# Kernel tuning notes

Measured on AMD Instinct MI355X. Metric: run time of the kernel, lower is better.

## Reference

```python
import jax, jax.numpy as jnp
import numpy as np
from jax import lax

N, C, H, W = 5, 256, 128, 128
RATIO = 16
KS = 3
SIGMA = 1.0
THRE = 0.01


def _conv2d_same(x, w):
    k = w.shape[-1]
    p = (k - 1) // 2
    return lax.conv_general_dilated(x, w, (1, 1), [(p, p), (p, p)],
                                    dimension_numbers=('NCHW', 'OIHW', 'NCHW'))


def _gaussian2d():
    c = KS // 2
    x, y = np.mgrid[-c:KS - c, -c:KS - c]
    g = 1.0 / (2.0 * np.pi * SIGMA) * np.exp(-(x ** 2 + y ** 2) / (2.0 * SIGMA ** 2))
    return jnp.asarray(g, jnp.float32).reshape(1, 1, KS, KS)


def _gaussian1d():
    x = np.arange(-(KS - 1) // 2, (KS + 1) // 2, dtype=np.float32)
    g = np.exp(-x ** 2 / (2.0 * SIGMA ** 2))
    g = g / g.sum()
    return jnp.asarray(g, jnp.float32).reshape(1, 1, KS)


def setup_inputs() -> dict:
    key = jax.random.key(0)
    ks = jax.random.split(key, 12)
    s = 0.05
    return {
        'feat': jax.random.normal(ks[0], (N, C, H, W), jnp.float32),
        'mlp_w1': jax.random.normal(ks[1], (C // RATIO, C), jnp.float32) * s,
        'mlp_w2': jax.random.normal(ks[2], (C, C // RATIO), jnp.float32) * s,
        'sp_req_w': jax.random.normal(ks[3], (1, 2, 3, 3), jnp.float32) * s,
        'ch_fus_w': jax.random.normal(ks[4], (C, 2 * C), jnp.float32) * s,
        'sp_fus_w': jax.random.normal(ks[5], (1, 2), jnp.float32) * s,
        'st_w1': jax.random.normal(ks[6], (4 * C, 2 * C), jnp.float32) * s,
        'st_b1': jax.random.normal(ks[7], (4 * C,), jnp.float32) * s,
        'st_w2': jax.random.normal(ks[8], (4 * C, 4 * C), jnp.float32) * s,
        'st_b2': jax.random.normal(ks[9], (4 * C,), jnp.float32) * s,
        'st_w3': jax.random.normal(ks[10], (1, 4 * C), jnp.float32) * s,
        'st_b3': jax.random.normal(ks[11], (1,), jnp.float32) * s,
    }


def _forward(feat, mlp_w1, mlp_w2, sp_req_w, ch_fus_w, sp_fus_w,
             st_w1, st_b1, st_w2, st_b2, st_w3, st_b3):
    g2 = _gaussian2d()
    g1 = _gaussian1d()

    # Channel_Request_Attention: shared MLP on avg- and max-pooled features
    avg = feat.mean(axis=(2, 3))          # [N, C]
    mx = feat.max(axis=(2, 3))            # [N, C]
    mlp = lambda v: jax.nn.relu(v @ mlp_w1.T) @ mlp_w2.T
    ch_att = jax.nn.sigmoid(mlp(avg) + mlp(mx))  # [N, C]

    # Spatial_Request_Attention: 3x3 conv over [mean, max] channel stats
    sp_in = jnp.concatenate([feat.mean(axis=1, keepdims=True),
                             feat.max(axis=1, keepdims=True)], axis=1)  # [N,2,H,W]
    sp_att = jax.nn.sigmoid(_conv2d_same(sp_in, sp_req_w))  # [N,1,H,W]

    # gaussian-smoothed activation map
    act = _conv2d_same(jax.nn.sigmoid(feat.mean(axis=1, keepdims=True)), g2)  # [N,1,H,W]

    ego_ch = 1.0 - ch_att[0]   # [C]
    ego_sp = 1.0 - sp_att[0]   # [1,H,W]

    # channel_fusion: 1x1 conv on concat([ego_request, collaborator_att]) -> split weight
    Wa, Wb = ch_fus_w[:, :C], ch_fus_w[:, C:]
    ch_coef = jax.nn.sigmoid(ego_ch @ Wa.T + ch_att[1:] @ Wb.T)  # [N-1, C]
    # smooth over the channel axis with 1D gaussian
    ch_coef = lax.conv_general_dilated(ch_coef[:, None, :], g1, (1,), [(KS // 2, KS // 2)],
                                       dimension_numbers=('NCH', 'OIH', 'NCH'))[:, 0, :]

    # spatial_fusion: 1x1 conv on concat([ego_sp_request, collaborator_sp_att])
    wa, wb = sp_fus_w[0, 0], sp_fus_w[0, 1]
    sp_coef = jax.nn.sigmoid(wa * ego_sp[None] + wb * sp_att[1:])  # [N-1,1,H,W]
    sp_coef = _conv2d_same(sp_coef, g2)

    sparse_matrix = ch_coef[:, :, None, None] * sp_coef * act[1:]  # [N-1,C,H,W]
    mask = (sparse_matrix > THRE).astype(feat.dtype)
    mean_rate = mask.mean()  # equal-sized per-collaborator means -> global mean

    sparse_feature = jnp.concatenate([feat[:1], feat[1:] * mask], axis=0)  # [N,C,H,W]
    sparse_mask = jnp.concatenate([jnp.ones_like(feat[:1]), mask], axis=0)

    def stat(x):
        h = jax.nn.relu(jnp.einsum('nchw,oc->nohw', x, st_w1) + st_b1[None, :, None, None])
        h = jax.nn.relu(jnp.einsum('nchw,oc->nohw', h, st_w2) + st_b2[None, :, None, None])
        return jnp.einsum('nchw,oc->nohw', h, st_w3) + st_b3[None, :, None, None]

    T = stat(jnp.concatenate([feat, sparse_feature], axis=1))
    feat_prime = jnp.roll(feat, -1, axis=0)
    T_prime = stat(jnp.concatenate([feat_prime, sparse_feature], axis=1))

    joint = (-jax.nn.softplus(-T)).mean()
    marginal = jax.nn.softplus(T_prime).mean()
    total_loss = -(joint - marginal)

    return sparse_feature, total_loss, mean_rate, sparse_mask


def reference(feat, mlp_w1, mlp_w2, sp_req_w, ch_fus_w, sp_fus_w,
              st_w1, st_b1, st_w2, st_b2, st_w3, st_b3):
    return _forward(feat, mlp_w1, mlp_w2, sp_req_w, ch_fus_w, sp_fus_w,
                    st_w1, st_b1, st_w2, st_b2, st_w3, st_b3)
```

## Files before the change

### kernel.cpp

```cpp
#include <hip/hip_runtime.h>
#include <cmath>

#define NIMG 5
#define CCH  256
#define HHH  128
#define WWW  128
#define HW   16384
#define NPIX 81920
#define SF_ELEMS 20971520
#define LOSS_OFF 20971520
#define RATE_OFF 20971521
#define MASK_OFF 20971522

typedef __attribute__((ext_vector_type(4))) float f32x4;
typedef __attribute__((ext_vector_type(8))) __bf16 bf16x8;
typedef __attribute__((ext_vector_type(8))) unsigned short u16x8;

__device__ __forceinline__ unsigned short f32_to_bf16(float f) {
  unsigned int u = __float_as_uint(f);
  u += 0x7FFFu + ((u >> 16) & 1u);
  return (unsigned short)(u >> 16);
}

__device__ __forceinline__ double sigmoid_d(double x) { return 1.0 / (1.0 + exp(-x)); }

__device__ __forceinline__ float softplus_f(float x) {
  if (x > 20.f) return x;
  if (x < -20.f) return expf(x);
  return log1pf(expf(x));
}

__device__ __forceinline__ double g2w(int ky, int kx) {
  int d2 = (ky - 1) * (ky - 1) + (kx - 1) * (kx - 1);
  double g = 0.15915494309189535 * exp(-0.5 * (double)d2);
  return (double)(float)g;
}

__device__ __forceinline__ void gload16(const unsigned short* g, void* l) {
  __builtin_amdgcn_global_load_lds((const __attribute__((address_space(1))) void*)g,
                                   (__attribute__((address_space(3))) void*)l, 16, 0, 0);
}

__global__ void k0_init(double* S1, double* S2, unsigned long long* cnt) {
  if (threadIdx.x == 0 && blockIdx.x == 0) { *S1 = 0.0; *S2 = 0.0; *cnt = 0ull; }
}

__global__ void k1_rednc(const float* __restrict__ feat, double* __restrict__ avg_d,
                         double* __restrict__ mx_d) {
  int nc = blockIdx.x;
  int t = threadIdx.x;
  const float* p = feat + (size_t)nc * HW;
  double s = 0.0;
  float m = -3.4e38f;
  for (int i = t; i < HW; i += 256) { float v = p[i]; s += (double)v; m = fmaxf(m, v); }
  __shared__ double sd[256];
  __shared__ float sm[256];
  sd[t] = s; sm[t] = m;
  __syncthreads();
  for (int o = 128; o > 0; o >>= 1) {
    if (t < o) { sd[t] += sd[t + o]; sm[t] = fmaxf(sm[t], sm[t + o]); }
    __syncthreads();
  }
  if (t == 0) { avg_d[nc] = sd[0] / 16384.0; mx_d[nc] = (double)sm[0]; }
}

__global__ void k2_rednp(const float* __restrict__ feat, double* __restrict__ chmean,
                         double* __restrict__ chmax) {
  int gid = blockIdx.x * 256 + threadIdx.x;
  int n = gid >> 14, p = gid & (HW - 1);
  const float* base = feat + (size_t)n * CCH * HW + p;
  double s = 0.0;
  float m = -3.4e38f;
  for (int c = 0; c < CCH; ++c) { float v = base[(size_t)c * HW]; s += (double)v; m = fmaxf(m, v); }
  chmean[gid] = s / 256.0;
  chmax[gid] = (double)m;
}

__global__ void k3_chan(const double* __restrict__ avg_d, const double* __restrict__ mx_d,
                        const float* __restrict__ w1, const float* __restrict__ w2,
                        const float* __restrict__ fus, double* __restrict__ chcoef_d) {
  __shared__ double hid_a[NIMG][16], hid_m[NIMG][16];
  __shared__ double att[NIMG][CCH];
  __shared__ double sig[4][CCH];
  int t = threadIdx.x;
  if (t < NIMG * 16) {
    int n = t / 16, j = t % 16;
    double sa = 0.0, sx = 0.0;
    for (int c = 0; c < CCH; ++c) {
      double w = (double)w1[j * CCH + c];
      sa += avg_d[n * CCH + c] * w;
      sx += mx_d[n * CCH + c] * w;
    }
    hid_a[n][j] = sa > 0.0 ? sa : 0.0;
    hid_m[n][j] = sx > 0.0 ? sx : 0.0;
  }
  __syncthreads();
  for (int n = 0; n < NIMG; ++n) {
    double oa = 0.0, om = 0.0;
    for (int j = 0; j < 16; ++j) {
      double w = (double)w2[t * 16 + j];
      oa += hid_a[n][j] * w;
      om += hid_m[n][j] * w;
    }
    att[n][t] = sigmoid_d(oa + om);
  }
  __syncthreads();
  for (int m = 0; m < 4; ++m) {
    double s = 0.0;
    for (int k = 0; k < CCH; ++k) {
      s += (1.0 - att[0][k]) * (double)fus[t * 512 + k]
         + att[m + 1][k] * (double)fus[t * 512 + 256 + k];
    }
    sig[m][t] = sigmoid_d(s);
  }
  __syncthreads();
  float a32 = (float)exp(-0.5);
  float s32 = (a32 + 1.0f) + a32;
  double ge = (double)(a32 / s32);
  double gc = (double)(1.0f / s32);
  for (int m = 0; m < 4; ++m) {
    double L = (t > 0) ? sig[m][t - 1] : 0.0;
    double R = (t < 255) ? sig[m][t + 1] : 0.0;
    chcoef_d[m * CCH + t] = ge * L + gc * sig[m][t] + ge * R;
  }
}

__global__ void k4_spatial(const double* __restrict__ chmean, const double* __restrict__ chmax,
                           const float* __restrict__ spw, double* __restrict__ spatt,
                           double* __restrict__ actb) {
  int gid = blockIdx.x * 256 + threadIdx.x;
  int n = gid >> 14, p = gid & (HW - 1);
  int y = p >> 7, x = p & 127;
  const double* cm = chmean + (size_t)n * HW;
  const double* cx = chmax + (size_t)n * HW;
  double s = 0.0, a = 0.0;
  for (int ky = 0; ky < 3; ++ky) {
    int yy = y + ky - 1;
    if ((unsigned)yy >= 128u) continue;
    for (int kx = 0; kx < 3; ++kx) {
      int xx = x + kx - 1;
      if ((unsigned)xx >= 128u) continue;
      int q = (yy << 7) + xx;
      s += (double)spw[ky * 3 + kx] * cm[q] + (double)spw[9 + ky * 3 + kx] * cx[q];
      a += g2w(ky, kx) * sigmoid_d(cm[q]);
    }
  }
  spatt[gid] = sigmoid_d(s);
  actb[gid] = a;
}

__global__ void k5a_spsig(const double* __restrict__ spatt, const float* __restrict__ fus2,
                          double* __restrict__ spsig) {
  int gid = blockIdx.x * 256 + threadIdx.x;
  int m = gid >> 14, p = gid & (HW - 1);
  double wa = (double)fus2[0], wb = (double)fus2[1];
  double ego = 1.0 - spatt[p];
  spsig[gid] = sigmoid_d(wa * ego + wb * spatt[(size_t)(m + 1) * HW + p]);
}

__global__ void k5b_spcoef(const double* __restrict__ spsig, const double* __restrict__ actb,
                           double* __restrict__ spact) {
  int gid = blockIdx.x * 256 + threadIdx.x;
  int m = gid >> 14, p = gid & (HW - 1);
  int y = p >> 7, x = p & 127;
  const double* sp = spsig + (size_t)m * HW;
  double s = 0.0;
  for (int ky = 0; ky < 3; ++ky) {
    int yy = y + ky - 1;
    if ((unsigned)yy >= 128u) continue;
    for (int kx = 0; kx < 3; ++kx) {
      int xx = x + kx - 1;
      if ((unsigned)xx >= 128u) continue;
      s += g2w(ky, kx) * sp[(yy << 7) + xx];
    }
  }
  spact[gid] = s * actb[(size_t)(m + 1) * HW + p];
}

__global__ void k6_mask(const float* __restrict__ feat, const double* __restrict__ chcoef,
                        const double* __restrict__ spact, float* __restrict__ out_sf,
                        float* __restrict__ out_mask, unsigned long long* __restrict__ cnt) {
  const int nth = gridDim.x * blockDim.x;
  int cl = 0;
  for (int g4 = blockIdx.x * blockDim.x + threadIdx.x; g4 < SF_ELEMS / 4; g4 += nth) {
    size_t e = (size_t)g4 * 4;
    int nc = (int)(e >> 14);
    int p = (int)(e & (HW - 1));
    int n = nc >> 8, c = nc & 255;
    f32x4 v = __builtin_nontemporal_load((const f32x4*)&feat[e]);
    f32x4 mk;
    if (n == 0) {
      mk = (f32x4){1.f, 1.f, 1.f, 1.f};
    } else {
      double cc = chcoef[(n - 1) * CCH + c];
      const double* sp = &spact[(size_t)(n - 1) * HW + p];
#pragma unroll
      for (int l = 0; l < 4; ++l) {
        float m = (cc * sp[l] > 0.01) ? 1.f : 0.f;
        mk[l] = m;
        cl += (m != 0.f);
      }
    }
    f32x4 o;
#pragma unroll
    for (int l = 0; l < 4; ++l) o[l] = v[l] * mk[l];
    __builtin_nontemporal_store(o, (f32x4*)&out_sf[e]);
    __builtin_nontemporal_store(mk, (f32x4*)&out_mask[e]);
  }
#pragma unroll
  for (int off = 32; off > 0; off >>= 1) cl += __shfl_down(cl, off);
  if ((threadIdx.x & 63) == 0 && cl > 0) atomicAdd(cnt, (unsigned long long)cl);
}

__global__ void k7_wconv(const float* __restrict__ w1, const float* __restrict__ w2,
                         unsigned short* __restrict__ W1b, unsigned short* __restrict__ W2b) {
  int gid = blockIdx.x * 256 + threadIdx.x;
  if (gid < 524288) W1b[gid] = f32_to_bf16(w1[gid]);
  W2b[gid] = f32_to_bf16(w2[gid]);
}

__global__ void k6b_transpose(const float* __restrict__ feat, const float* __restrict__ sf,
                              unsigned short* __restrict__ featT, unsigned short* __restrict__ sfT) {
  __shared__ unsigned short tf[64][65];
  __shared__ unsigned short tsb[64][65];
  const int bid = blockIdx.x;
  const int n  = bid >> 10;
  const int r  = bid & 1023;
  const int ct = r >> 8;
  const int pt = r & 255;
  const int c0 = ct << 6, p0 = pt << 6;
  const int t = threadIdx.x;
  {
    const int cy = t >> 2, px4 = (t & 3) << 4;
    const float* fp = feat + ((size_t)n * 256 + c0 + cy) * HW + p0 + px4;
    const float* sp = sf   + ((size_t)n * 256 + c0 + cy) * HW + p0 + px4;
#pragma unroll
    for (int i = 0; i < 4; ++i) {
      f32x4 v = *(const f32x4*)(fp + i * 4);
      f32x4 u = *(const f32x4*)(sp + i * 4);
#pragma unroll
      for (int j = 0; j < 4; ++j) {
        tf[cy][px4 + i * 4 + j]  = f32_to_bf16(v[j]);
        tsb[cy][px4 + i * 4 + j] = f32_to_bf16(u[j]);
      }
    }
  }
  __syncthreads();
  {
    const int py = t >> 2, cx = (t & 3) << 4;
    u16x8 o0, o1, q0, q1;
#pragma unroll
    for (int k = 0; k < 8; ++k) { o0[k] = tf[cx + k][py];     q0[k] = tsb[cx + k][py]; }
#pragma unroll
    for (int k = 0; k < 8; ++k) { o1[k] = tf[cx + 8 + k][py]; q1[k] = tsb[cx + 8 + k][py]; }
    size_t ob = ((size_t)n * HW + p0 + py) * 256 + c0 + cx;
    *(u16x8*)&featT[ob]     = o0;
    *(u16x8*)&featT[ob + 8] = o1;
    *(u16x8*)&sfT[ob]       = q0;
    *(u16x8*)&sfT[ob + 8]   = q1;
  }
}

__global__ void kT0_zero(float* __restrict__ T) {
  int g = blockIdx.x * 256 + threadIdx.x;
  for (int i = g; i < 163840; i += gridDim.x * 256) T[i] = 0.f;
}

template<int NT, bool L1>
__global__ __launch_bounds__(256, 2) void k8_gemm(
    const unsigned short* __restrict__ A0,
    const unsigned short* __restrict__ A1,
    const unsigned short* __restrict__ Wb,
    const float* __restrict__ bias,
    const float* __restrict__ w3,
    unsigned short* __restrict__ H1,
    float* __restrict__ Tout,
    int m_base) {
  __shared__ unsigned short lds[16384];

  const int bid0 = blockIdx.x;
  const int sb = (bid0 & 7) * 320 + (bid0 >> 3);
  const int mt = sb >> 3, nt = sb & 7;

  const int t = threadIdx.x, l = t & 63, w = t >> 6;
  const int wr = w >> 1, wc = w & 1;
  const int n16 = l & 15, quad = l >> 4;
  constexpr int ldb = L1 ? 512 : 1024;

  const unsigned short* base_feat = nullptr;
  const unsigned short* base_sf = nullptr;
  const unsigned short* base_a = nullptr;
  if constexpr (L1) {
    const int g0 = m_base + mt * 128;
    const int branch = (g0 >= NPIX) ? 1 : 0;
    const int rl = g0 - branch * NPIX;
    const int img = rl >> 14;
    const int p0 = rl & (HW - 1);
    const int img_f = branch ? (img + 1 == NIMG ? 0 : img + 1) : img;
    base_feat = A0 + ((size_t)img_f * HW + p0) * 256;
    base_sf   = A1 + ((size_t)img   * HW + p0) * 256;
  } else {
    base_a = A0 + (size_t)(mt * 128) * 1024;
  }
  const unsigned short* base_b = Wb + (size_t)(nt * 128) * ldb;

  const int r0 = l >> 2;
  const int kk = (l & 3) * 8;

  auto stage = [&](int buf, int ts) {
    const unsigned short* Ap;
    size_t as;
    if constexpr (L1) {
      if (ts < 8) { Ap = base_feat + ts * 32; } else { Ap = base_sf + (ts - 8) * 32; }
      as = 256;
    } else {
      Ap = base_a + ts * 32;
      as = 1024;
    }
    const unsigned short* Bp = base_b + ts * 32;
#pragma unroll
    for (int j = 0; j < 2; ++j) {
      const int s = w * 2 + j;
      gload16(Ap + (size_t)(s * 16 + r0) * as + kk, (void*)&lds[buf * 4096 + s * 512]);
      gload16(Bp + (size_t)(s * 16 + r0) * (size_t)ldb + kk, (void*)&lds[8192 + buf * 4096 + s * 512]);
    }
  };

  f32x4 acc[4][4];
  {
    f32x4 z = {0.f, 0.f, 0.f, 0.f};
#pragma unroll
    for (int g = 0; g < 4; ++g)
#pragma unroll
      for (int j = 0; j < 4; ++j) acc[g][j] = z;
  }

  stage(0, 0);
  for (int ts = 0; ts < NT; ++ts) {
    const int cur = ts & 1;
    if (ts + 1 < NT) {
      stage(cur ^ 1, ts + 1);
      asm volatile("s_waitcnt vmcnt(4)" ::: "memory");
    } else {
      asm volatile("s_waitcnt vmcnt(0)" ::: "memory");
    }
    asm volatile("s_barrier" ::: "memory");

    const int abase = cur * 4096 + (wr * 64) * 32;
    const int bbase = 8192 + cur * 4096 + (wc * 64) * 32;
    bf16x8 af[4], bg[4];
#pragma unroll
    for (int g = 0; g < 4; ++g) af[g] = *(const bf16x8*)&lds[abase + (g * 16 + n16) * 32 + quad * 8];
#pragma unroll
    for (int j = 0; j < 4; ++j) bg[j] = *(const bf16x8*)&lds[bbase + (j * 16 + n16) * 32 + quad * 8];
#pragma unroll
    for (int g = 0; g < 4; ++g)
#pragma unroll
      for (int j = 0; j < 4; ++j)
        acc[g][j] = __builtin_amdgcn_mfma_f32_16x16x32_bf16(af[g], bg[j], acc[g][j], 0, 0, 0);

    asm volatile("s_waitcnt lgkmcnt(0)" ::: "memory");
    asm volatile("s_barrier" ::: "memory");
  }

  const int colb = nt * 128 + wc * 64;
  if constexpr (L1) {
    const size_t mloc0 = (size_t)(mt * 128 + wr * 64);
#pragma unroll
    for (int j = 0; j < 4; ++j) {
      const int col = colb + j * 16 + n16;
      const float bv = bias[col];
#pragma unroll
      for (int g = 0; g < 4; ++g) {
#pragma unroll
        for (int rr = 0; rr < 4; ++rr) {
          float v = acc[g][j][rr] + bv;
          v = v > 0.f ? v : 0.f;
          H1[(mloc0 + g * 16 + quad * 4 + rr) * 1024 + col] = f32_to_bf16(v);
        }
      }
    }
  } else {
    float rs[4][4];
#pragma unroll
    for (int g = 0; g < 4; ++g)
#pragma unroll
      for (int rr = 0; rr < 4; ++rr) rs[g][rr] = 0.f;
#pragma unroll
    for (int j = 0; j < 4; ++j) {
      const int col = colb + j * 16 + n16;
      const float bv = bias[col];
      const float wv = w3[col];
#pragma unroll
      for (int g = 0; g < 4; ++g) {
#pragma unroll
        for (int rr = 0; rr < 4; ++rr) {
          float v = acc[g][j][rr] + bv;
          v = v > 0.f ? v : 0.f;
          rs[g][rr] += v * wv;
        }
      }
    }
#pragma unroll
    for (int off = 1; off < 16; off <<= 1) {
#pragma unroll
      for (int g = 0; g < 4; ++g)
#pragma unroll
        for (int rr = 0; rr < 4; ++rr) rs[g][rr] += __shfl_xor(rs[g][rr], off);
    }
    if (n16 == 0) {
      const int row0 = m_base + mt * 128 + wr * 64;
#pragma unroll
      for (int g = 0; g < 4; ++g)
#pragma unroll
        for (int rr = 0; rr < 4; ++rr)
          atomicAdd(&Tout[row0 + g * 16 + quad * 4 + rr], rs[g][rr]);
    }
  }
}

__global__ void k8c_red(const float* __restrict__ T, const float* __restrict__ b3,
                        double* __restrict__ S1, double* __restrict__ S2) {
  const int gid = blockIdx.x * 256 + threadIdx.x;
  const int stride = gridDim.x * 256;
  const float bv = b3[0];
  double s1 = 0.0, s2 = 0.0;
  for (int r = gid; r < 163840; r += stride) {
    float Tv = T[r] + bv;
    if (r < NPIX) s1 += (double)softplus_f(-Tv);
    else          s2 += (double)softplus_f(Tv);
  }
#pragma unroll
  for (int off = 32; off > 0; off >>= 1) {
    s1 += __shfl_down(s1, off);
    s2 += __shfl_down(s2, off);
  }
  __shared__ double l1[4], l2[4];
  const int wv = threadIdx.x >> 6;
  if ((threadIdx.x & 63) == 0) { l1[wv] = s1; l2[wv] = s2; }
  __syncthreads();
  if (threadIdx.x == 0) {
    atomicAdd(S1, l1[0] + l1[1] + l1[2] + l1[3]);
    atomicAdd(S2, l2[0] + l2[1] + l2[2] + l2[3]);
  }
}

__device__ __forceinline__ int xidx(int row, int c) {
  return row * 512 + ((((c >> 3) ^ (row & 7)) << 3) | (c & 7));
}
__device__ __forceinline__ int hidx(int row, int oc) {
  return 32768 + row * 256 + ((((oc >> 3) ^ (row & 7)) << 3) | (oc & 7));
}

__global__ __launch_bounds__(1024, 4) void k8_stat(
    const float* __restrict__ feat, const float* __restrict__ sf,
    const unsigned short* __restrict__ W1b, const unsigned short* __restrict__ W2b,
    const float* __restrict__ b1, const float* __restrict__ b2,
    const float* __restrict__ w3, const float* __restrict__ b3,
    double* __restrict__ S1, double* __restrict__ S2) {
  __shared__ unsigned short lds[49280];
  float* t_acc = (float*)&lds[49152];

  const int bid = blockIdx.x;
  const int n = bid >> 9;
  const int p0 = (bid & 511) << 5;
  const int n1 = (n + 1 == NIMG) ? 0 : n + 1;

  const int t = threadIdx.x;
  const int lane = t & 63;
  const int w = t >> 6;
  const int n16 = lane & 15;
  const int quad = lane >> 4;

  {
    const int c = t & 511;
    const int half = t >> 9;
    if (t < 64) t_acc[t] = 0.f;
#pragma unroll
    for (int rb = 0; rb < 2; ++rb) {
      const float* s = (c < 256)
          ? feat + ((size_t)(rb ? n1 : n) * CCH + c) * HW + p0
          : sf + ((size_t)n * CCH + (c - 256)) * HW + p0;
      const f32x4* s4 = (const f32x4*)(s + half * 16);
#pragma unroll
      for (int i = 0; i < 4; ++i) {
        f32x4 v = __builtin_nontemporal_load(s4 + i);
        const int prow = rb * 32 + half * 16 + i * 4;
#pragma unroll
        for (int l = 0; l < 4; ++l) lds[xidx(prow + l, c)] = f32_to_bf16(v[l]);
      }
    }
  }
  __syncthreads();

  f32x4 acc2[4][4];
  {
    f32x4 z = {0.f, 0.f, 0.f, 0.f};
#pragma unroll
    for (int g = 0; g < 4; ++g)
#pragma unroll
      for (int jt = 0; jt < 4; ++jt) acc2[g][jt] = z;
  }

  for (int nc = 0; nc < 4; ++nc) {
    f32x4 acc1[4];
    {
      f32x4 z = {0.f, 0.f, 0.f, 0.f};
#pragma unroll
      for (int g = 0; g < 4; ++g) acc1[g] = z;
    }
    const int o = nc * 256 + w * 16 + n16;
    const unsigned short* Wrow = W1b + (size_t)o * 512;
    bf16x8 bnxt = *(const bf16x8*)&Wrow[quad * 8];
    for (int ks = 0; ks < 16; ++ks) {
      bf16x8 b = bnxt;
      if (ks < 15) bnxt = *(const bf16x8*)&Wrow[(ks + 1) * 32 + quad * 8];
      const int cb = ks * 32 + quad * 8;
#pragma unroll
      for (int g = 0; g < 4; ++g) {
        bf16x8 a = *(const bf16x8*)&lds[xidx(g * 16 + n16, cb)];
        acc1[g] = __builtin_amdgcn_mfma_f32_16x16x32_bf16(a, b, acc1[g], 0, 0, 0);
      }
    }
    __syncthreads();

    {
      const float bv = b1[o];
      const int ol = w * 16 + n16;
#pragma unroll
      for (int g = 0; g < 4; ++g) {
#pragma unroll
        for (int r = 0; r < 4; ++r) {
          const int row = g * 16 + quad * 4 + r;
          float v = acc1[g][r] + bv;
          v = v > 0.f ? v : 0.f;
          lds[hidx(row, ol)] = f32_to_bf16(v);
        }
      }
    }
    __syncthreads();

    for (int ksl = 0; ksl < 8; ++ksl) {
      const int ocb = ksl * 32 + quad * 8;
      bf16x8 a[4];
#pragma unroll
      for (int g = 0; g < 4; ++g) a[g] = *(const bf16x8*)&lds[hidx(g * 16 + n16, ocb)];
#pragma unroll
      for (int jt = 0; jt < 4; ++jt) {
        const int o2 = w * 64 + jt * 16 + n16;
        bf16x8 b = *(const bf16x8*)&W2b[(size_t)o2 * 1024 + nc * 256 + ocb];
#pragma unroll
        for (int g = 0; g < 4; ++g)
          acc2[g][jt] = __builtin_amdgcn_mfma_f32_16x16x32_bf16(a[g], b, acc2[g][jt], 0, 0, 0);
      }
    }
  }

  float tp[4][4];
#pragma unroll
  for (int g = 0; g < 4; ++g)
#pragma unroll
    for (int r = 0; r < 4; ++r) tp[g][r] = 0.f;
#pragma unroll
  for (int jt = 0; jt < 4; ++jt) {
    const int o2 = w * 64 + jt * 16 + n16;
    const float bv = b2[o2];
    const float wv = w3[o2];
#pragma unroll
    for (int g = 0; g < 4; ++g) {
#pragma unroll
      for (int r = 0; r < 4; ++r) {
        float v = acc2[g][jt][r] + bv;
        v = v > 0.f ? v : 0.f;
        tp[g][r] += v * wv;
      }
    }
  }
#pragma unroll
  for (int off = 1; off < 16; off <<= 1) {
#pragma unroll
    for (int g = 0; g < 4; ++g)
#pragma unroll
      for (int r = 0; r < 4; ++r) tp[g][r] += __shfl_xor(tp[g][r], off);
  }
  if (n16 == 0) {
#pragma unroll
    for (int g = 0; g < 4; ++g)
#pragma unroll
      for (int r = 0; r < 4; ++r) atomicAdd(&t_acc[g * 16 + quad * 4 + r], tp[g][r]);
  }
  __syncthreads();

  if (t < 64) {
    const float T = t_acc[t] + b3[0];
    float v = (t < 32) ? softplus_f(-T) : softplus_f(T);
#pragma unroll
    for (int off = 16; off > 0; off >>= 1) v += __shfl_down(v, off);
    if (t == 0) atomicAdd(S1, (double)v);
    if (t == 32) atomicAdd(S2, (double)v);
  }
}

__global__ void k9_final(const double* __restrict__ S1, const double* __restrict__ S2,
                         const unsigned long long* __restrict__ cnt, float* __restrict__ out) {
  if (threadIdx.x == 0 && blockIdx.x == 0) {
    out[LOSS_OFF] = (float)(((*S1) + (*S2)) / 81920.0);
    out[RATE_OFF] = (float)((double)(*cnt) / 16777216.0);
  }
}

#define WS_FEATT 8388608ull
#define WS_SFT   50331648ull
#define WS_H1    92274688ull
#define WS_T     176160768ull
#define WS_NEED  176816128ull

extern "C" void kernel_launch(void* const* d_in, const int* in_sizes, int n_in,
                              void* d_out, int out_size, void* d_ws, size_t ws_size,
                              hipStream_t stream) {
  const float* feat     = (const float*)d_in[0];
  const float* mlp_w1   = (const float*)d_in[1];
  const float* mlp_w2   = (const float*)d_in[2];
  const float* sp_req_w = (const float*)d_in[3];
  const float* ch_fus_w = (const float*)d_in[4];
  const float* sp_fus_w = (const float*)d_in[5];
  const float* st_w1    = (const float*)d_in[6];
  const float* st_b1    = (const float*)d_in[7];
  const float* st_w2    = (const float*)d_in[8];
  const float* st_b2    = (const float*)d_in[9];
  const float* st_w3    = (const float*)d_in[10];
  const float* st_b3    = (const float*)d_in[11];
  float* out = (float*)d_out;

  char* ws = (char*)d_ws;
  double* S1     = (double*)(ws + 0);
  double* S2     = (double*)(ws + 8);
  unsigned long long* cnt = (unsigned long long*)(ws + 16);
  double* avg_d  = (double*)(ws + 64);
  double* mx_d   = (double*)(ws + 10304);
  double* chmean = (double*)(ws + 20544);
  double* chmax  = (double*)(ws + 675904);
  double* spatt  = (double*)(ws + 1331264);
  double* actb   = (double*)(ws + 1986624);
  double* chcoef = (double*)(ws + 2652224);
  double* spsig  = (double*)(ws + 2660416);
  double* spact  = (double*)(ws + 3184704);
  unsigned short* W1b = (unsigned short*)(ws + 3708992);
  unsigned short* W2b = (unsigned short*)(ws + 4757568);

  k0_init<<<1, 64, 0, stream>>>(S1, S2, cnt);
  k1_rednc<<<1280, 256, 0, stream>>>(feat, avg_d, mx_d);
  k2_rednp<<<320, 256, 0, stream>>>(feat, chmean, chmax);
  k3_chan<<<1, 256, 0, stream>>>(avg_d, mx_d, mlp_w1, mlp_w2, ch_fus_w, chcoef);
  k4_spatial<<<320, 256, 0, stream>>>(chmean, chmax, sp_req_w, spatt, actb);
  k5a_spsig<<<256, 256, 0, stream>>>(spatt, sp_fus_w, spsig);
  k5b_spcoef<<<256, 256, 0, stream>>>(spsig, actb, spact);
  k7_wconv<<<4096, 256, 0, stream>>>(st_w1, st_w2, W1b, W2b);
  k6_mask<<<2048, 256, 0, stream>>>(feat, chcoef, spact, out, out + MASK_OFF, cnt);

  if (ws_size >= WS_NEED) {
    unsigned short* featT = (unsigned short*)(ws + WS_FEATT);
    unsigned short* sfT   = (unsigned short*)(ws + WS_SFT);
    unsigned short* H1    = (unsigned short*)(ws + WS_H1);
    float* Tb             = (float*)(ws + WS_T);
    k6b_transpose<<<5120, 256, 0, stream>>>(feat, out, featT, sfT);
    kT0_zero<<<160, 256, 0, stream>>>(Tb);
    for (int c = 0; c < 4; ++c) {
      k8_gemm<16, true><<<2560, 256, 0, stream>>>(featT, sfT, W1b, st_b1, nullptr, H1, nullptr, c * 40960);
      k8_gemm<32, false><<<2560, 256, 0, stream>>>(H1, nullptr, W2b, st_b2, st_w3, nullptr, Tb, c * 40960);
    }
    k8c_red<<<160, 256, 0, stream>>>(Tb, st_b3, S1, S2);
  } else {
    k8_stat<<<2560, 1024, 0, stream>>>(feat, out, W1b, W2b, st_b1, st_b2, st_w3, st_b3, S1, S2);
  }

  k9_final<<<1, 64, 0, stream>>>(S1, S2, cnt, out);
}
```

Before: 1.157 ms.

## Fuse mask generation into bf16 transpose kernel and raise GEMM occupancy bound

The separate mask kernel is folded into the transpose kernel. Each block now computes the mask from the channel and spatial coefficients, writes the sparse feature and mask outputs, and produces the bf16 transposed copies in the same pass. This removes one full read of feat and the re-read of the sparse feature from global memory, with the nonzero count reduced per block before the atomic add. Separately, the GEMM launch bound goes from 2 to 4 blocks per SM, which may force register spilling.

```diff
diff --git a/kernel.cpp b/kernel.cpp
--- a/kernel.cpp
+++ b/kernel.cpp
@@ -219,10 +219,13 @@
   W2b[gid] = f32_to_bf16(w2[gid]);
 }
 
-__global__ void k6b_transpose(const float* __restrict__ feat, const float* __restrict__ sf,
-                              unsigned short* __restrict__ featT, unsigned short* __restrict__ sfT) {
+__global__ void k6bm(const float* __restrict__ feat, const double* __restrict__ chcoef,
+                     const double* __restrict__ spact, float* __restrict__ out_sf,
+                     float* __restrict__ out_mask, unsigned long long* __restrict__ cnt,
+                     unsigned short* __restrict__ featT, unsigned short* __restrict__ sfT) {
   __shared__ unsigned short tf[64][65];
   __shared__ unsigned short tsb[64][65];
+  __shared__ int cw[4];
   const int bid = blockIdx.x;
   const int n  = bid >> 10;
   const int r  = bid & 1023;
@@ -230,22 +233,50 @@
   const int pt = r & 255;
   const int c0 = ct << 6, p0 = pt << 6;
   const int t = threadIdx.x;
+  int cl = 0;
   {
     const int cy = t >> 2, px4 = (t & 3) << 4;
-    const float* fp = feat + ((size_t)n * 256 + c0 + cy) * HW + p0 + px4;
-    const float* sp = sf   + ((size_t)n * 256 + c0 + cy) * HW + p0 + px4;
+    const int c = c0 + cy;
+    const size_t eb = ((size_t)n * CCH + c) * HW + p0 + px4;
+    const float* fp = feat + eb;
+    double cc = 0.0;
+    const double* sp = nullptr;
+    if (n > 0) {
+      cc = chcoef[(n - 1) * CCH + c];
+      sp = spact + (size_t)(n - 1) * HW + p0 + px4;
+    }
 #pragma unroll
     for (int i = 0; i < 4; ++i) {
-      f32x4 v = *(const f32x4*)(fp + i * 4);
-      f32x4 u = *(const f32x4*)(sp + i * 4);
+      f32x4 v = __builtin_nontemporal_load((const f32x4*)(fp + i * 4));
+      f32x4 mk, o;
+      if (n == 0) {
+        mk = (f32x4){1.f, 1.f, 1.f, 1.f};
+      } else {
+#pragma unroll
+        for (int j = 0; j < 4; ++j) {
+          float m = (cc * sp[i * 4 + j] > 0.01) ? 1.f : 0.f;
+          mk[j] = m;
+          cl += (m != 0.f);
+        }
+      }
 #pragma unroll
       for (int j = 0; j < 4; ++j) {
+        o[j] = v[j] * mk[j];
         tf[cy][px4 + i * 4 + j]  = f32_to_bf16(v[j]);
-        tsb[cy][px4 + i * 4 + j] = f32_to_bf16(u[j]);
-      }
-    }
-  }
+        tsb[cy][px4 + i * 4 + j] = f32_to_bf16(o[j]);
+      }
+      __builtin_nontemporal_store(o, (f32x4*)(out_sf + eb + i * 4));
+      __builtin_nontemporal_store(mk, (f32x4*)(out_mask + eb + i * 4));
+    }
+  }
+#pragma unroll
+  for (int off = 32; off > 0; off >>= 1) cl += __shfl_down(cl, off);
+  if ((t & 63) == 0) cw[t >> 6] = cl;
   __syncthreads();
+  if (t == 0) {
+    int s = cw[0] + cw[1] + cw[2] + cw[3];
+    if (s > 0) atomicAdd(cnt, (unsigned long long)s);
+  }
   {
     const int py = t >> 2, cx = (t & 3) << 4;
     u16x8 o0, o1, q0, q1;
@@ -267,7 +298,7 @@
 }
 
 template<int NT, bool L1>
-__global__ __launch_bounds__(256, 2) void k8_gemm(
+__global__ __launch_bounds__(256, 4) void k8_gemm(
     const unsigned short* __restrict__ A0,
     const unsigned short* __restrict__ A1,
     const unsigned short* __restrict__ Wb,
@@ -656,14 +687,13 @@
   k5a_spsig<<<256, 256, 0, stream>>>(spatt, sp_fus_w, spsig);
   k5b_spcoef<<<256, 256, 0, stream>>>(spsig, actb, spact);
   k7_wconv<<<4096, 256, 0, stream>>>(st_w1, st_w2, W1b, W2b);
-  k6_mask<<<2048, 256, 0, stream>>>(feat, chcoef, spact, out, out + MASK_OFF, cnt);
 
   if (ws_size >= WS_NEED) {
     unsigned short* featT = (unsigned short*)(ws + WS_FEATT);
     unsigned short* sfT   = (unsigned short*)(ws + WS_SFT);
     unsigned short* H1    = (unsigned short*)(ws + WS_H1);
     float* Tb             = (float*)(ws + WS_T);
-    k6b_transpose<<<5120, 256, 0, stream>>>(feat, out, featT, sfT);
+    k6bm<<<5120, 256, 0, stream>>>(feat, chcoef, spact, out, out + MASK_OFF, cnt, featT, sfT);
     kT0_zero<<<160, 256, 0, stream>>>(Tb);
     for (int c = 0; c < 4; ++c) {
       k8_gemm<16, true><<<2560, 256, 0, stream>>>(featT, sfT, W1b, st_b1, nullptr, H1, nullptr, c * 40960);
@@ -671,6 +701,7 @@
     }
     k8c_red<<<160, 256, 0, stream>>>(Tb, st_b3, S1, S2);
   } else {
+    k6_mask<<<2048, 256, 0, stream>>>(feat, chcoef, spact, out, out + MASK_OFF, cnt);
     k8_stat<<<2560, 1024, 0, stream>>>(feat, out, W1b, W2b, st_b1, st_b2, st_w3, st_b3, S1, S2);
   }
 
```

After: 1.284 ms. 11.0% more time.
